# Kernel optimization log

Hardware: AMD Instinct MI355X
Metric: run time of the kernel (lower is better)

Reference implementation:

```python
import jax, jax.numpy as jnp
import numpy as np

NUM_HEADS = 16
Q_HEAD_DIM = 128
KV_HEAD_DIM = 128
ROPE_DIM = 64
LATENT_DIM = 512
INPUT_DIM = 2048


def setup_inputs() -> dict:
    key = jax.random.key(0)
    ks = jax.random.split(key, 7)
    B, S, D = 2, 2048, INPUT_DIM
    x = jax.random.normal(ks[0], (B, S, D), dtype=jnp.float32)
    positions = jnp.arange(S, dtype=jnp.int32)
    # weights stored as (in, out); torch Linear computes x @ W.T with W:(out,in)
    sc = lambda fan_in: 1.0 / np.sqrt(fan_in)
    Wq = jax.random.normal(ks[1], (D, NUM_HEADS * Q_HEAD_DIM), dtype=jnp.float32) * sc(D)
    Wc = jax.random.normal(ks[2], (D, LATENT_DIM), dtype=jnp.float32) * sc(D)
    Wk = jax.random.normal(ks[3], (LATENT_DIM, NUM_HEADS * KV_HEAD_DIM), dtype=jnp.float32) * sc(LATENT_DIM)
    Wv = jax.random.normal(ks[4], (LATENT_DIM, NUM_HEADS * KV_HEAD_DIM), dtype=jnp.float32) * sc(LATENT_DIM)
    Wo = jax.random.normal(ks[5], (NUM_HEADS * KV_HEAD_DIM, D), dtype=jnp.float32) * sc(NUM_HEADS * KV_HEAD_DIM)
    return {"x": x, "positions": positions, "Wq": Wq, "Wc": Wc, "Wk": Wk, "Wv": Wv, "Wo": Wo}


def _apply_rope_q(q, positions):
    # partial RoPE on first ROPE_DIM dims of q: (B,S,H,Dq)
    half = ROPE_DIM // 2
    inv_freq = 1.0 / (10000.0 ** (jnp.arange(0, ROPE_DIM, 2, dtype=jnp.float32) / ROPE_DIM))
    freqs = positions.astype(jnp.float32)[:, None] * inv_freq[None, :]  # (S, half)
    cos = jnp.cos(freqs)[None, :, None, :]  # (1,S,1,half)
    sin = jnp.sin(freqs)[None, :, None, :]
    x1 = q[..., :half]
    x2 = q[..., half:ROPE_DIM]
    rotated = jnp.concatenate([x1 * cos - x2 * sin, x1 * sin + x2 * cos], axis=-1)
    return jnp.concatenate([rotated, q[..., ROPE_DIM:]], axis=-1)


def reference(x, positions, Wq, Wc, Wk, Wv, Wo):
    B, S, _ = x.shape
    H, Dq, Dk = NUM_HEADS, Q_HEAD_DIM, KV_HEAD_DIM
    q = (x @ Wq).reshape(B, S, H, Dq)
    kv_latent = x @ Wc                       # (B,S,latent) low-rank compression
    k = (kv_latent @ Wk).reshape(B, S, H, Dk)
    v = (kv_latent @ Wv).reshape(B, S, H, Dk)
    q = _apply_rope_q(q, positions)          # RoPE applied to q only (as in source)
    scale = 1.0 / jnp.sqrt(jnp.float32(Dq))
    scores = jnp.einsum("bqhd,bkhd->bhqk", q, k) * scale
    attn = jax.nn.softmax(scores, axis=-1)
    out = jnp.einsum("bhqk,bkhd->bqhd", attn, v).reshape(B, S, H * Dk)
    return out @ Wo
```

## Files before the change

kernel.cpp:

```cpp
#include <hip/hip_runtime.h>
#include <math.h>


typedef __attribute__((ext_vector_type(8))) short bf16x8;
typedef __attribute__((ext_vector_type(4))) float f32x4;
typedef __attribute__((ext_vector_type(16))) float f32x16;

#define GLDS(gp, lp)                                                         \
  __builtin_amdgcn_global_load_lds(                                          \
      (const __attribute__((address_space(1))) void*)(gp),                   \
      (__attribute__((address_space(3))) void*)(lp), 16, 0, 0)

__device__ __forceinline__ short f2bf(float f) {
  unsigned u = __builtin_bit_cast(unsigned, f);
  u += 0x7fffu + ((u >> 16) & 1u);
  return (short)(u >> 16);
}
__device__ __forceinline__ float b2f(short x) {
  unsigned u = ((unsigned)(unsigned short)x) << 16;
  return __builtin_bit_cast(float, u);
}
__device__ __forceinline__ unsigned cvtpk(float lo, float hi) {
  unsigned r;
  asm("v_cvt_pk_bf16_f32 %0, %1, %2" : "=v"(r) : "v"(lo), "v"(hi));
  return r;
}

__global__ void cast4_kernel(const float* __restrict__ x, short* __restrict__ xb, int n4) {
  int i = blockIdx.x * blockDim.x + threadIdx.x;
  if (i < n4) {
    float4 v = ((const float4*)x)[i];
    ushort4 o;
    o.x = (unsigned short)f2bf(v.x);
    o.y = (unsigned short)f2bf(v.y);
    o.z = (unsigned short)f2bf(v.z);
    o.w = (unsigned short)f2bf(v.w);
    ((ushort4*)xb)[i] = o;
  }
}

__global__ void transpose_cast2_kernel(const float* __restrict__ W0, short* __restrict__ T0,
                                       const float* __restrict__ W1, short* __restrict__ T1,
                                       int K, int N) {
  const float* W = blockIdx.z ? W1 : W0;
  short* Wt = blockIdx.z ? T1 : T0;
  __shared__ float tile[32][33];
  int n0 = blockIdx.x * 32, k0 = blockIdx.y * 32;
  int tx = threadIdx.x & 31, ty = threadIdx.x >> 5;
#pragma unroll
  for (int i = 0; i < 4; ++i)
    tile[ty + i * 8][tx] = W[(size_t)(k0 + ty + i * 8) * N + n0 + tx];
  __syncthreads();
#pragma unroll
  for (int i = 0; i < 4; ++i)
    Wt[(size_t)(n0 + ty + i * 8) * K + k0 + tx] = f2bf(tile[tx][ty + i * 8]);
}

__global__ void rope_tab_kernel(const int* __restrict__ pos, float* __restrict__ cosT,
                                float* __restrict__ sinT) {
  int idx = blockIdx.x * 256 + threadIdx.x;
  if (idx < 2048 * 32) {
    int s = idx >> 5, i = idx & 31;
    float p = (float)pos[s];
    float freq = p * powf(10000.0f, -(float)(2 * i) / 64.0f);
    float sv, cv;
    sincosf(freq, &sv, &cv);
    cosT[idx] = cv;
    sinT[idx] = sv;
  }
}

template <int MODE>
__device__ __forceinline__ void gemm_core(const short* __restrict__ A,
                                          const short* __restrict__ Bt,
                                          void* __restrict__ Cv,
                                          int N, int K, int bm, int bn,
                                          short* sm) {
  const int tid  = threadIdx.x;
  const int lane = tid & 63;
  const int w    = tid >> 6;
  const int col  = lane & 15, g = lane >> 4;
  const int wr = w >> 1, wc = w & 1;

  f32x4 zero4 = {0.f, 0.f, 0.f, 0.f};
  f32x4 acc[4][4];
#pragma unroll
  for (int m = 0; m < 4; ++m)
#pragma unroll
    for (int n = 0; n < 4; ++n) acc[m][n] = zero4;

  const int sr = tid >> 3;
  const int sk = tid & 7;

  auto STAGE = [&](int buf, int t) {
#pragma unroll
    for (int i = 0; i < 4; ++i) {
      int r = i * 32 + sr;
      int c = (sk ^ (r & 7)) << 3;
      GLDS(A  + (size_t)(bm + r) * K + t * 64 + c,
           sm + buf * 8192 + i * 2048 + w * 512);
      GLDS(Bt + (size_t)(bn + r) * K + t * 64 + c,
           sm + 16384 + buf * 8192 + i * 2048 + w * 512);
    }
  };

  const int nt = K >> 6;
  STAGE(0, 0);
  __syncthreads();
  int buf = 0;
  for (int t = 0; t < nt; ++t) {
    if (t + 1 < nt) STAGE(buf ^ 1, t + 1);
    const short* As = sm + buf * 8192;
    const short* Bs = sm + 16384 + buf * 8192;
#pragma unroll
    for (int kk = 0; kk < 2; ++kk) {
      bf16x8 la[4], lb[4];
#pragma unroll
      for (int m = 0; m < 4; ++m) {
        int row = wr * 64 + m * 16 + col;
        la[m] = *(const bf16x8*)(As + row * 64 + (((kk * 4 + g) ^ (row & 7)) << 3));
      }
#pragma unroll
      for (int n = 0; n < 4; ++n) {
        int row = wc * 64 + n * 16 + col;
        lb[n] = *(const bf16x8*)(Bs + row * 64 + (((kk * 4 + g) ^ (row & 7)) << 3));
      }
#pragma unroll
      for (int m = 0; m < 4; ++m)
#pragma unroll
        for (int n = 0; n < 4; ++n)
          acc[m][n] = __builtin_amdgcn_mfma_f32_16x16x32_bf16(la[m], lb[n], acc[m][n], 0, 0, 0);
    }
    __syncthreads();
    buf ^= 1;
  }

  const int orow0 = bm + wr * 64;
  const int ocol0 = bn + wc * 64;
  if (MODE == 0) {
    short* C = (short*)Cv;
#pragma unroll
    for (int m = 0; m < 4; ++m)
#pragma unroll
      for (int n = 0; n < 4; ++n)
#pragma unroll
        for (int r = 0; r < 4; ++r)
          C[(size_t)(orow0 + m * 16 + g * 4 + r) * N + ocol0 + n * 16 + col] =
              f2bf(acc[m][n][r]);
  } else if (MODE == 1) {
    float* C = (float*)Cv;
#pragma unroll
    for (int m = 0; m < 4; ++m)
#pragma unroll
      for (int n = 0; n < 4; ++n)
#pragma unroll
        for (int r = 0; r < 4; ++r)
          C[(size_t)(orow0 + m * 16 + g * 4 + r) * N + ocol0 + n * 16 + col] =
              acc[m][n][r];
  } else {
    short* C = (short*)Cv;
#pragma unroll
    for (int m = 0; m < 4; ++m)
#pragma unroll
      for (int n = 0; n < 4; ++n) {
        int grow = orow0 + m * 16 + g * 4;
        int bb = grow >> 11, s = grow & 2047;
        int cn = ocol0 + n * 16 + col;
        ushort4 pk;
        pk.x = (unsigned short)f2bf(acc[m][n][0]);
        pk.y = (unsigned short)f2bf(acc[m][n][1]);
        pk.z = (unsigned short)f2bf(acc[m][n][2]);
        pk.w = (unsigned short)f2bf(acc[m][n][3]);
        *(ushort4*)(C + ((size_t)(bb * 2048 + cn)) * 2048 + s) = pk;
      }
  }
}

__global__ __launch_bounds__(256, 2) void gemm_qc(const short* __restrict__ xb,
                                                  const short* __restrict__ wqT,
                                                  const short* __restrict__ wcT,
                                                  short* __restrict__ qb,
                                                  short* __restrict__ kvb) {
  __shared__ alignas(16) short sm[32768];
  int x = blockIdx.x, y = blockIdx.y;
  if (x < 16) gemm_core<0>(xb, wqT, qb, 2048, 2048, y * 128, x * 128, sm);
  else        gemm_core<0>(xb, wcT, kvb, 512, 2048, y * 128, (x - 16) * 128, sm);
}
__global__ __launch_bounds__(256, 2) void gemm_kv(const short* __restrict__ kvb,
                                                  const short* __restrict__ wkT,
                                                  const short* __restrict__ wvT,
                                                  short* __restrict__ kb,
                                                  short* __restrict__ vtb) {
  __shared__ alignas(16) short sm[32768];
  int x = blockIdx.x, y = blockIdx.y;
  if (x < 16) gemm_core<0>(kvb, wkT, kb, 2048, 512, y * 128, x * 128, sm);
  else        gemm_core<2>(kvb, wvT, vtb, 2048, 512, y * 128, (x - 16) * 128, sm);
}
__global__ __launch_bounds__(256, 2) void gemm_wo(const short* __restrict__ obuf,
                                                  const short* __restrict__ woT,
                                                  float* __restrict__ out) {
  __shared__ alignas(16) short sm[32768];
  gemm_core<1>(obuf, woT, out, 2048, 2048, blockIdx.y * 128, blockIdx.x * 128, sm);
}

__global__ __launch_bounds__(256, 2) void attn_kernel(
    const short* __restrict__ qb, const short* __restrict__ kb,
    const short* __restrict__ vt, short* __restrict__ ob,
    const float* __restrict__ cosT, const float* __restrict__ sinT) {
  __shared__ alignas(16) short sm[32768];
  const int lane = threadIdx.x & 63, w = threadIdx.x >> 6;
  const int ql = lane & 31, hi = lane >> 5;
  const int qt = blockIdx.x >> 5, bh = blockIdx.x & 31;
  const int b = bh >> 4, h = bh & 15;
  const int q0w = qt * 128 + w * 32;
  const int qrow = q0w + ql;

  bf16x8 qf[8];
  {
    const short* qp = qb + ((size_t)(b * 2048 + qrow)) * 2048 + h * 128;
#pragma unroll
    for (int db = 0; db < 8; ++db) qf[db] = *(const bf16x8*)(qp + db * 16 + hi * 8);
    const float* cp = cosT + qrow * 32;
    const float* sp = sinT + qrow * 32;
#pragma unroll
    for (int db = 0; db < 2; ++db)
#pragma unroll
      for (int j = 0; j < 8; ++j) {
        int i = db * 16 + hi * 8 + j;
        float x1 = b2f(qf[db][j]), x2 = b2f(qf[db + 2][j]);
        float cv = cp[i], sv = sp[i];
        qf[db][j]     = f2bf(x1 * cv - x2 * sv);
        qf[db + 2][j] = f2bf(x1 * sv + x2 * cv);
      }
  }

  f32x16 o[4];
#pragma unroll
  for (int m4 = 0; m4 < 4; ++m4)
#pragma unroll
    for (int r = 0; r < 16; ++r) o[m4][r] = 0.f;
  float mrun = -3.0e38f, lrun = 0.f;

  auto STAGE = [&](int buf, int kt) {
#pragma unroll
    for (int i = 0; i < 4; ++i) {
      int r = w * 16 + i * 4 + (lane >> 4);
      int cch = lane & 15;
      const short* gp = kb + ((size_t)(b * 2048 + kt * 64 + r)) * 2048 + h * 128 +
                        ((cch ^ (r & 7)) << 3);
      GLDS(gp, sm + buf * 8192 + w * 2048 + i * 512);
    }
#pragma unroll
    for (int i = 0; i < 4; ++i) {
      int rd = w * 32 + i * 8 + (lane >> 3);
      int cch = lane & 7;
      const short* gp = vt + ((size_t)(b * 2048 + h * 128 + rd)) * 2048 + kt * 64 +
                        ((cch ^ (rd & 7)) << 3);
      GLDS(gp, sm + 16384 + buf * 8192 + w * 2048 + i * 512);
    }
  };

  const float cl2 = 0.12752744590518352f;
  STAGE(0, 0);
  __syncthreads();
  int buf = 0;
  for (int kt = 0; kt < 32; ++kt) {
    if (kt + 1 < 32) STAGE(buf ^ 1, kt + 1);
    const short* Ks = sm + buf * 8192;
    const short* Vs = sm + 16384 + buf * 8192;

    f32x16 skt[2];
    __builtin_amdgcn_s_setprio(1);
#pragma unroll
    for (int kb2 = 0; kb2 < 2; ++kb2) {
      f32x16 a;
#pragma unroll
      for (int r = 0; r < 16; ++r) a[r] = 0.f;
      int krow = kb2 * 32 + ql;
#pragma unroll
      for (int db = 0; db < 8; ++db) {
        bf16x8 kf = *(const bf16x8*)(Ks + krow * 128 + (((db * 2 + hi) ^ (krow & 7)) << 3));
        a = __builtin_amdgcn_mfma_f32_32x32x16_bf16(kf, qf[db], a, 0, 0, 0);
      }
      skt[kb2] = a;
    }
    __builtin_amdgcn_s_setprio(0);

#pragma unroll
    for (int kb2 = 0; kb2 < 2; ++kb2)
#pragma unroll
      for (int r = 0; r < 16; ++r) skt[kb2][r] *= cl2;

    float t0, t1, t2, t3;
    t0 = fmaxf(fmaxf(fmaxf(fmaxf(skt[0][0], skt[0][4]), skt[0][8]),
                     fmaxf(skt[0][12], skt[1][0])),
               fmaxf(fmaxf(skt[1][4], skt[1][8]), skt[1][12]));
    t1 = fmaxf(fmaxf(fmaxf(fmaxf(skt[0][1], skt[0][5]), skt[0][9]),
                     fmaxf(skt[0][13], skt[1][1])),
               fmaxf(fmaxf(skt[1][5], skt[1][9]), skt[1][13]));
    t2 = fmaxf(fmaxf(fmaxf(fmaxf(skt[0][2], skt[0][6]), skt[0][10]),
                     fmaxf(skt[0][14], skt[1][2])),
               fmaxf(fmaxf(skt[1][6], skt[1][10]), skt[1][14]));
    t3 = fmaxf(fmaxf(fmaxf(fmaxf(skt[0][3], skt[0][7]), skt[0][11]),
                     fmaxf(skt[0][15], skt[1][3])),
               fmaxf(fmaxf(skt[1][7], skt[1][11]), skt[1][15]));
    float tmax = fmaxf(fmaxf(t0, t1), fmaxf(t2, t3));
    tmax = fmaxf(tmax, __shfl_xor(tmax, 32));

    if (!__all(tmax <= mrun + 8.0f)) {
      float mn = fmaxf(mrun, tmax);
      float fr = __builtin_amdgcn_exp2f(mrun - mn);
      mrun = mn;
      lrun *= fr;
#pragma unroll
      for (int m4 = 0; m4 < 4; ++m4)
#pragma unroll
        for (int r = 0; r < 16; ++r) o[m4][r] *= fr;
    }
    float s0 = 0.f, s1 = 0.f, s2 = 0.f, s3 = 0.f;
#pragma unroll
    for (int kb2 = 0; kb2 < 2; ++kb2)
#pragma unroll
      for (int r = 0; r < 16; r += 4) {
        skt[kb2][r]     = __builtin_amdgcn_exp2f(skt[kb2][r] - mrun);
        skt[kb2][r + 1] = __builtin_amdgcn_exp2f(skt[kb2][r + 1] - mrun);
        skt[kb2][r + 2] = __builtin_amdgcn_exp2f(skt[kb2][r + 2] - mrun);
        skt[kb2][r + 3] = __builtin_amdgcn_exp2f(skt[kb2][r + 3] - mrun);
        s0 += skt[kb2][r];     s1 += skt[kb2][r + 1];
        s2 += skt[kb2][r + 2]; s3 += skt[kb2][r + 3];
      }
    float psum = (s0 + s1) + (s2 + s3);
    psum += __shfl_xor(psum, 32);
    lrun += psum;

    bf16x8 pf[4];
#pragma unroll
    for (int kb2 = 0; kb2 < 2; ++kb2) {
#pragma unroll
      for (int half = 0; half < 2; ++half) {
        unsigned a0 = cvtpk(skt[kb2][half * 8 + 0], skt[kb2][half * 8 + 1]);
        unsigned a1 = cvtpk(skt[kb2][half * 8 + 2], skt[kb2][half * 8 + 3]);
        unsigned b0 = cvtpk(skt[kb2][half * 8 + 4], skt[kb2][half * 8 + 5]);
        unsigned b1 = cvtpk(skt[kb2][half * 8 + 6], skt[kb2][half * 8 + 7]);
        unsigned pa0 = __shfl_xor(a0, 32), pa1 = __shfl_xor(a1, 32);
        unsigned pb0 = __shfl_xor(b0, 32), pb1 = __shfl_xor(b1, 32);
        union { unsigned u[4]; bf16x8 v; } tmp;
        tmp.u[0] = hi ? pb0 : a0;
        tmp.u[1] = hi ? pb1 : a1;
        tmp.u[2] = hi ? b0 : pa0;
        tmp.u[3] = hi ? b1 : pa1;
        pf[kb2 * 2 + half] = tmp.v;
      }
    }

    __builtin_amdgcn_s_setprio(1);
#pragma unroll
    for (int m4 = 0; m4 < 4; ++m4) {
      int rd = m4 * 32 + ql;
#pragma unroll
      for (int ks = 0; ks < 4; ++ks) {
        bf16x8 vf = *(const bf16x8*)(Vs + rd * 64 + (((ks * 2 + hi) ^ (rd & 7)) << 3));
        o[m4] = __builtin_amdgcn_mfma_f32_32x32x16_bf16(vf, pf[ks], o[m4], 0, 0, 0);
      }
    }
    __builtin_amdgcn_s_setprio(0);
    __syncthreads();
    buf ^= 1;
  }

  float il = 1.0f / lrun;
  short* E = sm + w * 4352;
#pragma unroll
  for (int m4 = 0; m4 < 4; ++m4)
#pragma unroll
    for (int r = 0; r < 16; r += 2) {
      int d = m4 * 32 + (r & 3) + 8 * (r >> 2) + 4 * hi;
      unsigned pk = cvtpk(o[m4][r] * il, o[m4][r + 1] * il);
      *(unsigned*)(E + ql * 136 + d) = pk;
    }
  asm volatile("s_waitcnt lgkmcnt(0)" ::: "memory");
#pragma unroll
  for (int it = 0; it < 8; ++it) {
    int row = it * 4 + (lane >> 4);
    int ch = lane & 15;
    bf16x8 v = *(const bf16x8*)(E + row * 136 + ch * 8);
    *(bf16x8*)(ob + ((size_t)(b * 2048 + q0w + row)) * 2048 + h * 128 + ch * 8) = v;
  }
}

extern "C" void kernel_launch(void* const* d_in, const int* in_sizes, int n_in,
                              void* d_out, int out_size, void* d_ws, size_t ws_size,
                              hipStream_t stream) {
  (void)in_sizes; (void)n_in; (void)out_size; (void)ws_size;
  const float* x  = (const float*)d_in[0];
  const int*   pos = (const int*)d_in[1];
  const float* Wq = (const float*)d_in[2];
  const float* Wc = (const float*)d_in[3];
  const float* Wk = (const float*)d_in[4];
  const float* Wv = (const float*)d_in[5];
  const float* Wo = (const float*)d_in[6];

  char* ws = (char*)d_ws;
  short* xb   = (short*)(ws);
  short* qb   = (short*)(ws + 16777216);
  short* kvb  = (short*)(ws + 33554432);
  short* kb   = (short*)(ws + 37748736);
  short* vtb  = (short*)(ws + 54525952);
  short* obuf = (short*)(ws + 71303168);
  short* wqT  = (short*)(ws + 88080384);
  short* wcT  = (short*)(ws + 96468992);
  short* wkT  = (short*)(ws + 98566144);
  short* wvT  = (short*)(ws + 100663296);
  short* woT  = (short*)(ws + 102760448);
  float* cosT = (float*)(ws + 111149056);
  float* sinT = (float*)(ws + 111411200);

  cast4_kernel<<<8192, 256, 0, stream>>>(x, xb, 2097152);
  transpose_cast2_kernel<<<dim3(64, 64, 2), 256, 0, stream>>>(Wq, wqT, Wo, woT, 2048, 2048);
  transpose_cast2_kernel<<<dim3(16, 64, 1), 256, 0, stream>>>(Wc, wcT, Wc, wcT, 2048, 512);
  transpose_cast2_kernel<<<dim3(64, 16, 2), 256, 0, stream>>>(Wk, wkT, Wv, wvT, 512, 2048);
  rope_tab_kernel<<<256, 256, 0, stream>>>(pos, cosT, sinT);

  gemm_qc<<<dim3(20, 32), 256, 0, stream>>>(xb, wqT, wcT, qb, kvb);
  gemm_kv<<<dim3(32, 32), 256, 0, stream>>>(kvb, wkT, wvT, kb, vtb);

  attn_kernel<<<512, 256, 0, stream>>>(qb, kb, vtb, obuf, cosT, sinT);

  gemm_wo<<<dim3(16, 32), 256, 0, stream>>>(obuf, woT, (float*)d_out);
}
```

Baseline: 232.0 us.

## Shrink attention tiles to 64 query rows and 32-key KV steps

The attention kernel now uses 2-wave blocks that each handle 64 query rows instead of 4-wave blocks handling 128. Key/value tiles shrink from 64 to 32 keys per step, and the LDS staging, swizzle and V-fragment addressing are reworked to match. The grid doubles to 1024 blocks with half the shared memory per block. The aim is better occupancy and load balance across CUs, at the cost of each K/V tile being reloaded by twice as many blocks and twice as many barrier-separated loop steps.

```diff
diff --git a/kernel.cpp b/kernel.cpp
--- a/kernel.cpp
+++ b/kernel.cpp
@@ -203,16 +203,17 @@
   gemm_core<1>(obuf, woT, out, 2048, 2048, blockIdx.y * 128, blockIdx.x * 128, sm);
 }
 
-__global__ __launch_bounds__(256, 2) void attn_kernel(
+__global__ __launch_bounds__(128, 2) void attn_kernel(
     const short* __restrict__ qb, const short* __restrict__ kb,
     const short* __restrict__ vt, short* __restrict__ ob,
     const float* __restrict__ cosT, const float* __restrict__ sinT) {
-  __shared__ alignas(16) short sm[32768];
-  const int lane = threadIdx.x & 63, w = threadIdx.x >> 6;
+  __shared__ alignas(16) short sm[16384];
+  const int tid = threadIdx.x;
+  const int lane = tid & 63, w = tid >> 6;
   const int ql = lane & 31, hi = lane >> 5;
   const int qt = blockIdx.x >> 5, bh = blockIdx.x & 31;
   const int b = bh >> 4, h = bh & 15;
-  const int q0w = qt * 128 + w * 32;
+  const int q0w = qt * 64 + w * 32;
   const int qrow = q0w + ql;
 
   bf16x8 qf[8];
@@ -244,19 +245,19 @@
   auto STAGE = [&](int buf, int kt) {
 #pragma unroll
     for (int i = 0; i < 4; ++i) {
-      int r = w * 16 + i * 4 + (lane >> 4);
-      int cch = lane & 15;
-      const short* gp = kb + ((size_t)(b * 2048 + kt * 64 + r)) * 2048 + h * 128 +
+      int r = i * 8 + (tid >> 4);
+      int cch = tid & 15;
+      const short* gp = kb + ((size_t)(b * 2048 + kt * 32 + r)) * 2048 + h * 128 +
                         ((cch ^ (r & 7)) << 3);
-      GLDS(gp, sm + buf * 8192 + w * 2048 + i * 512);
+      GLDS(gp, sm + buf * 4096 + i * 1024 + w * 512);
     }
 #pragma unroll
     for (int i = 0; i < 4; ++i) {
-      int rd = w * 32 + i * 8 + (lane >> 3);
-      int cch = lane & 7;
-      const short* gp = vt + ((size_t)(b * 2048 + h * 128 + rd)) * 2048 + kt * 64 +
-                        ((cch ^ (rd & 7)) << 3);
-      GLDS(gp, sm + 16384 + buf * 8192 + w * 2048 + i * 512);
+      int rd = i * 32 + (tid >> 2);
+      int cch = tid & 3;
+      const short* gp = vt + ((size_t)(b * 2048 + h * 128 + rd)) * 2048 + kt * 32 +
+                        ((cch ^ ((rd >> 1) & 3)) << 3);
+      GLDS(gp, sm + 8192 + buf * 4096 + i * 1024 + w * 512);
     }
   };
 
@@ -264,46 +265,31 @@
   STAGE(0, 0);
   __syncthreads();
   int buf = 0;
-  for (int kt = 0; kt < 32; ++kt) {
-    if (kt + 1 < 32) STAGE(buf ^ 1, kt + 1);
-    const short* Ks = sm + buf * 8192;
-    const short* Vs = sm + 16384 + buf * 8192;
-
-    f32x16 skt[2];
+  for (int kt = 0; kt < 64; ++kt) {
+    if (kt + 1 < 64) STAGE(buf ^ 1, kt + 1);
+    const short* Ks = sm + buf * 4096;
+    const short* Vs = sm + 8192 + buf * 4096;
+
+    f32x16 skt;
     __builtin_amdgcn_s_setprio(1);
-#pragma unroll
-    for (int kb2 = 0; kb2 < 2; ++kb2) {
+    {
       f32x16 a;
 #pragma unroll
       for (int r = 0; r < 16; ++r) a[r] = 0.f;
-      int krow = kb2 * 32 + ql;
 #pragma unroll
       for (int db = 0; db < 8; ++db) {
-        bf16x8 kf = *(const bf16x8*)(Ks + krow * 128 + (((db * 2 + hi) ^ (krow & 7)) << 3));
+        bf16x8 kf = *(const bf16x8*)(Ks + ql * 128 + (((db * 2 + hi) ^ (ql & 7)) << 3));
         a = __builtin_amdgcn_mfma_f32_32x32x16_bf16(kf, qf[db], a, 0, 0, 0);
       }
-      skt[kb2] = a;
+#pragma unroll
+      for (int r = 0; r < 16; ++r) skt[r] = a[r] * cl2;
     }
     __builtin_amdgcn_s_setprio(0);
 
-#pragma unroll
-    for (int kb2 = 0; kb2 < 2; ++kb2)
-#pragma unroll
-      for (int r = 0; r < 16; ++r) skt[kb2][r] *= cl2;
-
-    float t0, t1, t2, t3;
-    t0 = fmaxf(fmaxf(fmaxf(fmaxf(skt[0][0], skt[0][4]), skt[0][8]),
-                     fmaxf(skt[0][12], skt[1][0])),
-               fmaxf(fmaxf(skt[1][4], skt[1][8]), skt[1][12]));
-    t1 = fmaxf(fmaxf(fmaxf(fmaxf(skt[0][1], skt[0][5]), skt[0][9]),
-                     fmaxf(skt[0][13], skt[1][1])),
-               fmaxf(fmaxf(skt[1][5], skt[1][9]), skt[1][13]));
-    t2 = fmaxf(fmaxf(fmaxf(fmaxf(skt[0][2], skt[0][6]), skt[0][10]),
-                     fmaxf(skt[0][14], skt[1][2])),
-               fmaxf(fmaxf(skt[1][6], skt[1][10]), skt[1][14]));
-    t3 = fmaxf(fmaxf(fmaxf(fmaxf(skt[0][3], skt[0][7]), skt[0][11]),
-                     fmaxf(skt[0][15], skt[1][3])),
-               fmaxf(fmaxf(skt[1][7], skt[1][11]), skt[1][15]));
+    float t0 = fmaxf(fmaxf(skt[0], skt[4]), fmaxf(skt[8], skt[12]));
+    float t1 = fmaxf(fmaxf(skt[1], skt[5]), fmaxf(skt[9], skt[13]));
+    float t2 = fmaxf(fmaxf(skt[2], skt[6]), fmaxf(skt[10], skt[14]));
+    float t3 = fmaxf(fmaxf(skt[3], skt[7]), fmaxf(skt[11], skt[15]));
     float tmax = fmaxf(fmaxf(t0, t1), fmaxf(t2, t3));
     tmax = fmaxf(tmax, __shfl_xor(tmax, 32));
 
@@ -319,38 +305,32 @@
     }
     float s0 = 0.f, s1 = 0.f, s2 = 0.f, s3 = 0.f;
 #pragma unroll
-    for (int kb2 = 0; kb2 < 2; ++kb2)
-#pragma unroll
-      for (int r = 0; r < 16; r += 4) {
-        skt[kb2][r]     = __builtin_amdgcn_exp2f(skt[kb2][r] - mrun);
-        skt[kb2][r + 1] = __builtin_amdgcn_exp2f(skt[kb2][r + 1] - mrun);
-        skt[kb2][r + 2] = __builtin_amdgcn_exp2f(skt[kb2][r + 2] - mrun);
-        skt[kb2][r + 3] = __builtin_amdgcn_exp2f(skt[kb2][r + 3] - mrun);
-        s0 += skt[kb2][r];     s1 += skt[kb2][r + 1];
-        s2 += skt[kb2][r + 2]; s3 += skt[kb2][r + 3];
-      }
+    for (int r = 0; r < 16; r += 4) {
+      skt[r]     = __builtin_amdgcn_exp2f(skt[r] - mrun);
+      skt[r + 1] = __builtin_amdgcn_exp2f(skt[r + 1] - mrun);
+      skt[r + 2] = __builtin_amdgcn_exp2f(skt[r + 2] - mrun);
+      skt[r + 3] = __builtin_amdgcn_exp2f(skt[r + 3] - mrun);
+      s0 += skt[r]; s1 += skt[r + 1]; s2 += skt[r + 2]; s3 += skt[r + 3];
+    }
     float psum = (s0 + s1) + (s2 + s3);
     psum += __shfl_xor(psum, 32);
     lrun += psum;
 
-    bf16x8 pf[4];
-#pragma unroll
-    for (int kb2 = 0; kb2 < 2; ++kb2) {
-#pragma unroll
-      for (int half = 0; half < 2; ++half) {
-        unsigned a0 = cvtpk(skt[kb2][half * 8 + 0], skt[kb2][half * 8 + 1]);
-        unsigned a1 = cvtpk(skt[kb2][half * 8 + 2], skt[kb2][half * 8 + 3]);
-        unsigned b0 = cvtpk(skt[kb2][half * 8 + 4], skt[kb2][half * 8 + 5]);
-        unsigned b1 = cvtpk(skt[kb2][half * 8 + 6], skt[kb2][half * 8 + 7]);
-        unsigned pa0 = __shfl_xor(a0, 32), pa1 = __shfl_xor(a1, 32);
-        unsigned pb0 = __shfl_xor(b0, 32), pb1 = __shfl_xor(b1, 32);
-        union { unsigned u[4]; bf16x8 v; } tmp;
-        tmp.u[0] = hi ? pb0 : a0;
-        tmp.u[1] = hi ? pb1 : a1;
-        tmp.u[2] = hi ? b0 : pa0;
-        tmp.u[3] = hi ? b1 : pa1;
-        pf[kb2 * 2 + half] = tmp.v;
-      }
+    bf16x8 pf[2];
+#pragma unroll
+    for (int half = 0; half < 2; ++half) {
+      unsigned a0 = cvtpk(skt[half * 8 + 0], skt[half * 8 + 1]);
+      unsigned a1 = cvtpk(skt[half * 8 + 2], skt[half * 8 + 3]);
+      unsigned b0 = cvtpk(skt[half * 8 + 4], skt[half * 8 + 5]);
+      unsigned b1 = cvtpk(skt[half * 8 + 6], skt[half * 8 + 7]);
+      unsigned pa0 = __shfl_xor(a0, 32), pa1 = __shfl_xor(a1, 32);
+      unsigned pb0 = __shfl_xor(b0, 32), pb1 = __shfl_xor(b1, 32);
+      union { unsigned u[4]; bf16x8 v; } tmp;
+      tmp.u[0] = hi ? pb0 : a0;
+      tmp.u[1] = hi ? pb1 : a1;
+      tmp.u[2] = hi ? b0 : pa0;
+      tmp.u[3] = hi ? b1 : pa1;
+      pf[half] = tmp.v;
     }
 
     __builtin_amdgcn_s_setprio(1);
@@ -358,8 +338,8 @@
     for (int m4 = 0; m4 < 4; ++m4) {
       int rd = m4 * 32 + ql;
 #pragma unroll
-      for (int ks = 0; ks < 4; ++ks) {
-        bf16x8 vf = *(const bf16x8*)(Vs + rd * 64 + (((ks * 2 + hi) ^ (rd & 7)) << 3));
+      for (int ks = 0; ks < 2; ++ks) {
+        bf16x8 vf = *(const bf16x8*)(Vs + rd * 32 + (((ks * 2 + hi) ^ ((rd >> 1) & 3)) << 3));
         o[m4] = __builtin_amdgcn_mfma_f32_32x32x16_bf16(vf, pf[ks], o[m4], 0, 0, 0);
       }
     }
@@ -424,7 +404,7 @@
   gemm_qc<<<dim3(20, 32), 256, 0, stream>>>(xb, wqT, wcT, qb, kvb);
   gemm_kv<<<dim3(32, 32), 256, 0, stream>>>(kvb, wkT, wvT, kb, vtb);
 
-  attn_kernel<<<512, 256, 0, stream>>>(qb, kb, vtb, obuf, cosT, sinT);
+  attn_kernel<<<1024, 128, 0, stream>>>(qb, kb, vtb, obuf, cosT, sinT);
 
   gemm_wo<<<dim3(16, 32), 256, 0, stream>>>(obuf, woT, (float*)d_out);
 }
```

New measurement: 252.9 us. +9.0%, slower.
